# Kernel tuning notes

Hardware: AMD Instinct MI355X
Metric: run time of the kernel (lower is better)

Reference implementation:

```python
import jax, jax.numpy as jnp
import numpy as np

USER_NUM = 100000
ITEM_NUM = 50000
N_NODES = USER_NUM + ITEM_NUM
EMB = 64
NNZ = 6400000
N_LAYERS = 3
NORM_EPS = 1e-12
LEAKY_SLOPE = 0.01
DROP_P = 0.5


def setup_inputs() -> dict:
    key = jax.random.key(0)
    ks = jax.random.split(key, 8)
    return {
        "user_emb": jax.random.normal(ks[0], (USER_NUM, EMB), jnp.float32) * 0.1,
        "item_emb": jax.random.normal(ks[1], (ITEM_NUM, EMB), jnp.float32) * 0.1,
        "image_emb": jax.random.normal(ks[2], (ITEM_NUM, EMB), jnp.float32) * 0.1,
        "text_emb": jax.random.normal(ks[3], (ITEM_NUM, EMB), jnp.float32) * 0.1,
        "fusion_weight": jax.nn.softmax(jax.random.normal(ks[4], (3,), jnp.float32)),
        "adj_vals": jax.random.uniform(ks[5], (NNZ,), jnp.float32) * 0.01,
        "adj_rows": jax.random.randint(ks[6], (NNZ,), 0, N_NODES, jnp.int32),
        "adj_cols": jax.random.randint(ks[7], (NNZ,), 0, N_NODES, jnp.int32),
    }


def _l2norm(x):
    # F.normalize(x, p=2, dim=1) with clamp_min(1e-12)
    n = jnp.sqrt(jnp.sum(x * x, axis=1, keepdims=True))
    return x / jnp.maximum(n, NORM_EPS)


def reference(user_emb, item_emb, image_emb, text_emb, fusion_weight,
              adj_vals, adj_rows, adj_cols):
    def spmm(x):  # COO sparse @ dense: gather cols, scale, scatter-add rows
        return jax.ops.segment_sum(adj_vals[:, None] * x[adj_cols], adj_rows,
                                   num_segments=N_NODES)

    ego = jnp.concatenate([user_emb, item_emb], axis=0)   # [N, E]
    img = jnp.concatenate([user_emb, image_emb], axis=0)  # [N, E]
    txt = jnp.concatenate([user_emb, text_emb], axis=0)   # [N, E]

    dkey = jax.random.key(42)
    ego_acc = jnp.zeros_like(ego)
    img_acc = jnp.zeros_like(img)
    txt_acc = jnp.zeros_like(txt)
    for k in range(N_LAYERS):
        ego = spmm(ego)
        img = spmm(img)
        txt = spmm(txt)
        img = jax.nn.leaky_relu(img, LEAKY_SLOPE)
        txt = jax.nn.leaky_relu(txt, LEAKY_SLOPE)
        ki, kt = jax.random.split(jax.random.fold_in(dkey, k))
        img = jnp.where(jax.random.bernoulli(ki, 1.0 - DROP_P, img.shape),
                        img / (1.0 - DROP_P), 0.0)
        txt = jnp.where(jax.random.bernoulli(kt, 1.0 - DROP_P, txt.shape),
                        txt / (1.0 - DROP_P), 0.0)
        ego_acc = ego_acc + ego
        img_acc = img_acc + _l2norm(img)
        txt_acc = txt_acc + _l2norm(txt)

    inv_l = 1.0 / N_LAYERS
    fin_e = ego_acc * inv_l
    fin_i = img_acc * inv_l
    fin_t = txt_acc * inv_l

    user_all = fin_e[:USER_NUM]
    item_e = fin_e[USER_NUM:]
    item_i = fin_i[USER_NUM:]
    item_t = fin_t[USER_NUM:]
    w = fusion_weight
    item_all = w[0] * item_e + w[1] * item_i + w[2] * item_t
    return user_all, item_all
```

## Files before the change

### kernel.cpp

```cpp
#include <hip/hip_runtime.h>
#include <hip/hip_bf16.h>

#define USER_NUM 100000
#define N_NODES  150000
#define EMB      64
#define NNZ      6400000
#define MATF ((size_t)N_NODES * EMB)

#define RPB1   512
#define NB1    ((N_NODES + RPB1 - 1) / RPB1)
#define CHUNK1 4096
#define NCB    19
#define NCELL  (RPB1 * NCB)

__host__ __device__ __forceinline__ void tf_block(unsigned k0, unsigned k1,
                                                  unsigned x0, unsigned x1,
                                                  unsigned& o0, unsigned& o1) {
    unsigned ks[3] = {k0, k1, k0 ^ k1 ^ 0x1BD11BDAu};
    unsigned X0 = x0 + ks[0];
    unsigned X1 = x1 + ks[1];
    const int R[2][4] = {{13, 15, 26, 6}, {17, 29, 16, 24}};
#pragma unroll
    for (int i = 0; i < 5; ++i) {
        const int* r = R[i & 1];
#pragma unroll
        for (int j = 0; j < 4; ++j) {
            X0 += X1;
            X1 = (X1 << r[j]) | (X1 >> (32 - r[j]));
            X1 ^= X0;
        }
        X0 += ks[(i + 1) % 3];
        X1 += ks[(i + 2) % 3] + (unsigned)(i + 1);
    }
    o0 = X0; o1 = X1;
}

__device__ __forceinline__ unsigned short f_to_bfu(float f) {
    __hip_bfloat16 b = __float2bfloat16(f);
    return *(unsigned short*)&b;
}
__device__ __forceinline__ float bfu_to_f(unsigned short u) {
    return __uint_as_float((unsigned)u << 16);
}

#define BHIST_BLOCKS 2048
__global__ __launch_bounds__(256) void bhist_k(const int* __restrict__ rows,
                                               int* __restrict__ bb) {
    __shared__ int h[NB1];
    for (int i = threadIdx.x; i < NB1; i += 256) h[i] = 0;
    __syncthreads();
    const int stride = BHIST_BLOCKS * 256;
    for (int e = blockIdx.x * 256 + threadIdx.x; e < NNZ; e += stride)
        atomicAdd(&h[rows[e] >> 9], 1);
    __syncthreads();
    for (int i = threadIdx.x; i < NB1; i += 256)
        if (h[i]) atomicAdd(&bb[i], h[i]);
}

__global__ __launch_bounds__(512) void bscan_k(int* __restrict__ bb,
                                               int* __restrict__ bcur) {
    __shared__ int sh[512];
    int t = threadIdx.x;
    int v = (t < NB1) ? bb[t] : 0;
    sh[t] = v;
    __syncthreads();
    for (int off = 1; off < 512; off <<= 1) {
        int x = (t >= off) ? sh[t - off] : 0;
        __syncthreads();
        sh[t] += x;
        __syncthreads();
    }
    int ex = sh[t] - v;
    if (t < NB1) { bb[t] = ex; bcur[t] = ex; }
    if (t == NB1 - 1) bb[NB1] = sh[t];
}

__global__ __launch_bounds__(256) void p1_k(const int* __restrict__ rows,
                                            const int* __restrict__ cols,
                                            const float* __restrict__ vals,
                                            int* __restrict__ bcur,
                                            int2* __restrict__ tmp) {
    __shared__ int2 stage[CHUNK1];
    __shared__ unsigned short sb[CHUNK1];
    __shared__ int hist[NB1], lbase[NB1], lcur[NB1], gbase[NB1];
    const int tid = threadIdx.x;
    const int c0 = blockIdx.x * CHUNK1;
    const int n = (c0 + CHUNK1 <= NNZ) ? CHUNK1 : (NNZ - c0);

    for (int b = tid; b < NB1; b += 256) hist[b] = 0;
    __syncthreads();

    int2 pay[CHUNK1 / 256];
    int  pb[CHUNK1 / 256];
#pragma unroll
    for (int k = 0; k < CHUNK1 / 256; ++k) {
        int i = tid + k * 256;
        if (i < n) {
            int e = c0 + i;
            int r = rows[e];
            int b = r >> 9;
            pay[k] = make_int2(cols[e] | ((r & 511) << 18),
                               __float_as_int(vals[e]));
            pb[k] = b;
            atomicAdd(&hist[b], 1);
        } else pb[k] = -1;
    }
    __syncthreads();

    if (tid == 0) {
        int run = 0;
        for (int b = 0; b < NB1; ++b) {
            lbase[b] = run;
            lcur[b] = run;
            run += hist[b];
        }
    }
    __syncthreads();
    for (int b = tid; b < NB1; b += 256)
        if (hist[b] > 0) gbase[b] = atomicAdd(&bcur[b], hist[b]);
    __syncthreads();

#pragma unroll
    for (int k = 0; k < CHUNK1 / 256; ++k) {
        if (pb[k] >= 0) {
            int pos = atomicAdd(&lcur[pb[k]], 1);
            stage[pos] = pay[k];
            sb[pos] = (unsigned short)pb[k];
        }
    }
    __syncthreads();

    for (int i = tid; i < n; i += 256) {
        int b = sb[i];
        tmp[gbase[b] + (i - lbase[b])] = stage[i];
    }
}

__global__ __launch_bounds__(256) void p2_k(const int* __restrict__ bb,
                                            const int2* __restrict__ tmp,
                                            int2* __restrict__ edges,
                                            int* __restrict__ cur) {
    __shared__ int lh[NCELL];
    __shared__ int ps[256];
    int b = blockIdx.x;
    int tid = threadIdx.x;
    int base = bb[b];
    int cnt = bb[b + 1] - base;

    for (int i = tid; i < NCELL; i += 256) lh[i] = 0;
    __syncthreads();

    for (int i = tid; i < cnt; i += 256) {
        int x = tmp[base + i].x;
        int cell = ((x >> 18) & 511) * NCB + ((x & 0x3FFFF) >> 13);
        atomicAdd(&lh[cell], 1);
    }
    __syncthreads();

    const int PC = (NCELL + 255) / 256;
    int lo = tid * PC;
    int hi = lo + PC < NCELL ? lo + PC : NCELL;
    int s = 0;
    for (int i = lo; i < hi; ++i) s += lh[i];
    ps[tid] = s;
    __syncthreads();
    for (int off = 1; off < 256; off <<= 1) {
        int x = (tid >= off) ? ps[tid - off] : 0;
        __syncthreads();
        ps[tid] += x;
        __syncthreads();
    }
    int run = base + ps[tid] - s;
    for (int i = lo; i < hi; ++i) {
        int d = lh[i];
        lh[i] = run;
        run += d;
    }
    __syncthreads();

    for (int i = tid; i < cnt; i += 256) {
        int2 w = tmp[base + i];
        int cell = ((w.x >> 18) & 511) * NCB + ((w.x & 0x3FFFF) >> 13);
        int pos = atomicAdd(&lh[cell], 1);
        edges[pos] = make_int2(w.x & 0x3FFFF, w.y);
    }
    __syncthreads();

    int r0 = b * RPB1;
    for (int t = tid; t < RPB1; t += 256) {
        int r = r0 + t;
        if (r < N_NODES) cur[r] = lh[t * NCB + (NCB - 1)];
    }
}

__global__ __launch_bounds__(256) void pack0_k(
    const float* __restrict__ user, const float* __restrict__ item,
    const float* __restrict__ image, const float* __restrict__ text,
    unsigned short* __restrict__ pE, unsigned* __restrict__ pIT) {
    size_t idx = (size_t)blockIdx.x * 256 + threadIdx.x;
    if (idx >= MATF) return;
    int row = (int)(idx >> 6);
    float e, i, t;
    if (row < USER_NUM) {
        float u = user[idx];
        e = u; i = u; t = u;
    } else {
        size_t cc = idx - (size_t)USER_NUM * EMB;
        e = item[cc]; i = image[cc]; t = text[cc];
    }
    pE[idx]  = f_to_bfu(e);
    pIT[idx] = (unsigned)f_to_bfu(i) | ((unsigned)f_to_bfu(t) << 16);
}

__global__ __launch_bounds__(256) void spmm_post(
    const int* __restrict__ cur, const int2* __restrict__ edges,
    const unsigned short* __restrict__ sE, const unsigned* __restrict__ sIT,
    unsigned short* __restrict__ dE, unsigned* __restrict__ dIT,
    const float* __restrict__ w, float* __restrict__ out,
    unsigned ki0, unsigned ki1, unsigned kt0, unsigned kt1,
    int writeBack, int first) {
    int row = (int)((blockIdx.x * 256u + threadIdx.x) >> 6);
    int lane = threadIdx.x & 63;
    if (row >= N_NODES) return;
    int beg = __builtin_amdgcn_readfirstlane((row == 0) ? 0 : cur[row - 1]);
    int end = __builtin_amdgcn_readfirstlane(cur[row]);
    float ae = 0.f, ai = 0.f, at = 0.f;
#pragma unroll 8
    for (int i = beg; i < end; ++i) {
        int2 cv = edges[i];
        size_t cc = (size_t)cv.x * EMB + lane;
        float v = __int_as_float(cv.y);
        float xe = bfu_to_f(sE[cc]);
        unsigned it = sIT[cc];
        float xi = __uint_as_float(it << 16);
        float xt = __uint_as_float(it & 0xffff0000u);
        ae += v * xe; ai += v * xi; at += v * xt;
    }

    size_t idx = (size_t)row * EMB + lane;
    unsigned j = (unsigned)idx;

    float iv = ai >= 0.f ? ai : 0.01f * ai;
    float tv = at >= 0.f ? at : 0.01f * at;
    unsigned y0, y1;
    tf_block(ki0, ki1, 0u, j, y0, y1);
    iv = ((y0 ^ y1) >> 31) ? 0.f : iv * 2.f;
    tf_block(kt0, kt1, 0u, j, y0, y1);
    tv = ((y0 ^ y1) >> 31) ? 0.f : tv * 2.f;

    if (writeBack) {
        dE[idx]  = f_to_bfu(ae);
        dIT[idx] = (unsigned)f_to_bfu(iv) | ((unsigned)f_to_bfu(tv) << 16);
    }

    float si = iv * iv, st2 = tv * tv;
#pragma unroll
    for (int m = 1; m < 64; m <<= 1) {
        si  += __shfl_xor(si, m, 64);
        st2 += __shfl_xor(st2, m, 64);
    }
    float ni = iv / fmaxf(sqrtf(si), 1e-12f);
    float nt = tv / fmaxf(sqrtf(st2), 1e-12f);

    const float inv3 = 1.0f / 3.0f;
    float contrib = (row < USER_NUM) ? ae * inv3
                                     : (w[0] * ae + w[1] * ni + w[2] * nt) * inv3;
    if (first) out[idx] = contrib;
    else       out[idx] += contrib;
}

extern "C" void kernel_launch(void* const* d_in, const int* in_sizes, int n_in,
                              void* d_out, int out_size, void* d_ws, size_t ws_size,
                              hipStream_t stream) {
    const float* user  = (const float*)d_in[0];
    const float* item  = (const float*)d_in[1];
    const float* image = (const float*)d_in[2];
    const float* text  = (const float*)d_in[3];
    const float* w     = (const float*)d_in[4];
    const float* vals  = (const float*)d_in[5];
    const int*   rows  = (const int*)d_in[6];
    const int*   cols  = (const int*)d_in[7];
    float* out = (float*)d_out;

    int2* edges = (int2*)d_ws;
    unsigned short* eA = (unsigned short*)(edges + NNZ);
    unsigned short* eB = eA + MATF;
    unsigned* itA = (unsigned*)(eB + MATF);
    unsigned* itB = itA + MATF;
    int* cur  = (int*)(itB + MATF);
    int* bb   = cur + N_NODES;
    int* bcur = bb + (NB1 + 2);
    int2* tmp = (int2*)eB;

    hipMemsetAsync(bb, 0, (NB1 + 1) * sizeof(int), stream);
    bhist_k<<<BHIST_BLOCKS, 256, 0, stream>>>(rows, bb);
    bscan_k<<<1, 512, 0, stream>>>(bb, bcur);
    p1_k<<<(NNZ + CHUNK1 - 1) / CHUNK1, 256, 0, stream>>>(rows, cols, vals,
                                                          bcur, tmp);
    p2_k<<<NB1, 256, 0, stream>>>(bb, tmp, edges, cur);

    const int blocks = (int)((MATF + 255) / 256);
    pack0_k<<<blocks, 256, 0, stream>>>(user, item, image, text, eA, itA);

    unsigned short* sE = eA; unsigned* sIT = itA;
    unsigned short* dE = eB; unsigned* dIT = itB;
    for (int k = 0; k < 3; ++k) {
        unsigned f0, f1, a0, a1, b0, b1;
        tf_block(0u, 42u, 0u, (unsigned)k, f0, f1);
        tf_block(f0, f1, 0u, 0u, a0, a1);
        tf_block(f0, f1, 0u, 1u, b0, b1);
        int writeBack = (k < 2) ? 1 : 0;
        spmm_post<<<blocks, 256, 0, stream>>>(
            cur, edges, sE, sIT, dE, dIT, w, out, a0, a1, b0, b1,
            writeBack, k == 0 ? 1 : 0);
        unsigned short* te = sE; unsigned* tit = sIT;
        sE = dE; sIT = dIT;
        dE = te; dIT = tit;
    }
}
```

Baseline: 1.280 ms.

## Pack user and item inputs separately and add non-temporal edge/output accesses

The initial packing no longer builds concatenated ego/img/txt matrices. It stores the user rows once plus separate item, image and text buffers. The first SpMM layer is specialised to branch per column: a user column is gathered once into a single accumulator that is later added to all three channels. Edge loads and output and writeback stores become non-temporal hints to reduce cache pollution. The changes add a data-dependent branch in the first-layer inner loop and extra workspace, and the non-temporal hints may hurt if the data would have been reused.

After: 1.349 ms. 1.05x slower.

```diff
diff --git a/kernel.cpp b/kernel.cpp
--- a/kernel.cpp
+++ b/kernel.cpp
@@ -6,6 +6,8 @@
 #define EMB      64
 #define NNZ      6400000
 #define MATF ((size_t)N_NODES * EMB)
+#define UMATF ((size_t)USER_NUM * EMB)
+#define IMATF ((size_t)(N_NODES - USER_NUM) * EMB)
 
 #define RPB1   512
 #define NB1    ((N_NODES + RPB1 - 1) / RPB1)
@@ -196,46 +198,62 @@
 __global__ __launch_bounds__(256) void pack0_k(
     const float* __restrict__ user, const float* __restrict__ item,
     const float* __restrict__ image, const float* __restrict__ text,
-    unsigned short* __restrict__ pE, unsigned* __restrict__ pIT) {
+    unsigned short* __restrict__ pU, unsigned short* __restrict__ pIE,
+    unsigned* __restrict__ pIIT) {
     size_t idx = (size_t)blockIdx.x * 256 + threadIdx.x;
-    if (idx >= MATF) return;
-    int row = (int)(idx >> 6);
-    float e, i, t;
-    if (row < USER_NUM) {
-        float u = user[idx];
-        e = u; i = u; t = u;
-    } else {
-        size_t cc = idx - (size_t)USER_NUM * EMB;
-        e = item[cc]; i = image[cc]; t = text[cc];
-    }
-    pE[idx]  = f_to_bfu(e);
-    pIT[idx] = (unsigned)f_to_bfu(i) | ((unsigned)f_to_bfu(t) << 16);
-}
-
+    if (idx < UMATF) {
+        pU[idx] = f_to_bfu(user[idx]);
+    }
+    if (idx < IMATF) {
+        pIE[idx]  = f_to_bfu(item[idx]);
+        pIIT[idx] = (unsigned)f_to_bfu(image[idx]) |
+                    ((unsigned)f_to_bfu(text[idx]) << 16);
+    }
+}
+
+template <bool FIRST>
 __global__ __launch_bounds__(256) void spmm_post(
     const int* __restrict__ cur, const int2* __restrict__ edges,
     const unsigned short* __restrict__ sE, const unsigned* __restrict__ sIT,
+    const unsigned short* __restrict__ pU, const unsigned short* __restrict__ pIE,
+    const unsigned* __restrict__ pIIT,
     unsigned short* __restrict__ dE, unsigned* __restrict__ dIT,
     const float* __restrict__ w, float* __restrict__ out,
-    unsigned ki0, unsigned ki1, unsigned kt0, unsigned kt1,
-    int writeBack, int first) {
+    unsigned ki0, unsigned ki1, unsigned kt0, unsigned kt1, int writeBack) {
     int row = (int)((blockIdx.x * 256u + threadIdx.x) >> 6);
     int lane = threadIdx.x & 63;
     if (row >= N_NODES) return;
     int beg = __builtin_amdgcn_readfirstlane((row == 0) ? 0 : cur[row - 1]);
     int end = __builtin_amdgcn_readfirstlane(cur[row]);
-    float ae = 0.f, ai = 0.f, at = 0.f;
+    const long long* edges64 = (const long long*)edges;
+    float ae = 0.f, ai = 0.f, at = 0.f, su = 0.f;
 #pragma unroll 8
     for (int i = beg; i < end; ++i) {
-        int2 cv = edges[i];
-        size_t cc = (size_t)cv.x * EMB + lane;
-        float v = __int_as_float(cv.y);
-        float xe = bfu_to_f(sE[cc]);
-        unsigned it = sIT[cc];
-        float xi = __uint_as_float(it << 16);
-        float xt = __uint_as_float(it & 0xffff0000u);
-        ae += v * xe; ai += v * xi; at += v * xt;
-    }
+        long long cvp = __builtin_nontemporal_load(edges64 + i);
+        int c = (int)(unsigned)(cvp & 0xffffffffu);
+        float v = __uint_as_float((unsigned)((unsigned long long)cvp >> 32));
+        if (FIRST) {
+            if (c < USER_NUM) {
+                float u = bfu_to_f(pU[(size_t)c * EMB + lane]);
+                su += v * u;
+            } else {
+                size_t cc = (size_t)(c - USER_NUM) * EMB + lane;
+                float xe = bfu_to_f(pIE[cc]);
+                unsigned it = pIIT[cc];
+                ae += v * xe;
+                ai += v * __uint_as_float(it << 16);
+                at += v * __uint_as_float(it & 0xffff0000u);
+            }
+        } else {
+            size_t cc = (size_t)c * EMB + lane;
+            float xe = bfu_to_f(sE[cc]);
+            unsigned it = sIT[cc];
+            ae += v * xe;
+            ai += v * __uint_as_float(it << 16);
+            at += v * __uint_as_float(it & 0xffff0000u);
+        }
+    }
+    if (FIRST) { ae += su; ai += su; at += su; }
 
     size_t idx = (size_t)row * EMB + lane;
     unsigned j = (unsigned)idx;
@@ -249,8 +267,9 @@
     tv = ((y0 ^ y1) >> 31) ? 0.f : tv * 2.f;
 
     if (writeBack) {
-        dE[idx]  = f_to_bfu(ae);
-        dIT[idx] = (unsigned)f_to_bfu(iv) | ((unsigned)f_to_bfu(tv) << 16);
+        __builtin_nontemporal_store(f_to_bfu(ae), &dE[idx]);
+        __builtin_nontemporal_store(
+            (unsigned)f_to_bfu(iv) | ((unsigned)f_to_bfu(tv) << 16), &dIT[idx]);
     }
 
     float si = iv * iv, st2 = tv * tv;
@@ -265,8 +284,12 @@
     const float inv3 = 1.0f / 3.0f;
     float contrib = (row < USER_NUM) ? ae * inv3
                                      : (w[0] * ae + w[1] * ni + w[2] * nt) * inv3;
-    if (first) out[idx] = contrib;
-    else       out[idx] += contrib;
+    if (FIRST) {
+        __builtin_nontemporal_store(contrib, &out[idx]);
+    } else {
+        float o = __builtin_nontemporal_load(&out[idx]);
+        __builtin_nontemporal_store(o + contrib, &out[idx]);
+    }
 }
 
 extern "C" void kernel_launch(void* const* d_in, const int* in_sizes, int n_in,
@@ -287,7 +310,10 @@
     unsigned short* eB = eA + MATF;
     unsigned* itA = (unsigned*)(eB + MATF);
     unsigned* itB = itA + MATF;
-    int* cur  = (int*)(itB + MATF);
+    unsigned short* pU  = (unsigned short*)(itB + MATF);
+    unsigned short* pIE = pU + UMATF;
+    unsigned* pIIT = (unsigned*)(pIE + IMATF);
+    int* cur  = (int*)(pIIT + IMATF);
     int* bb   = cur + N_NODES;
     int* bcur = bb + (NB1 + 2);
     int2* tmp = (int2*)eB;
@@ -300,21 +326,26 @@
     p2_k<<<NB1, 256, 0, stream>>>(bb, tmp, edges, cur);
 
     const int blocks = (int)((MATF + 255) / 256);
-    pack0_k<<<blocks, 256, 0, stream>>>(user, item, image, text, eA, itA);
-
-    unsigned short* sE = eA; unsigned* sIT = itA;
-    unsigned short* dE = eB; unsigned* dIT = itB;
+    pack0_k<<<(int)((UMATF + 255) / 256), 256, 0, stream>>>(
+        user, item, image, text, pU, pIE, pIIT);
+
     for (int k = 0; k < 3; ++k) {
         unsigned f0, f1, a0, a1, b0, b1;
         tf_block(0u, 42u, 0u, (unsigned)k, f0, f1);
         tf_block(f0, f1, 0u, 0u, a0, a1);
         tf_block(f0, f1, 0u, 1u, b0, b1);
-        int writeBack = (k < 2) ? 1 : 0;
-        spmm_post<<<blocks, 256, 0, stream>>>(
-            cur, edges, sE, sIT, dE, dIT, w, out, a0, a1, b0, b1,
-            writeBack, k == 0 ? 1 : 0);
-        unsigned short* te = sE; unsigned* tit = sIT;
-        sE = dE; sIT = dIT;
-        dE = te; dIT = tit;
-    }
-}
+        if (k == 0) {
+            spmm_post<true><<<blocks, 256, 0, stream>>>(
+                cur, edges, nullptr, nullptr, pU, pIE, pIIT,
+                eA, itA, w, out, a0, a1, b0, b1, 1);
+        } else if (k == 1) {
+            spmm_post<false><<<blocks, 256, 0, stream>>>(
+                cur, edges, eA, itA, nullptr, nullptr, nullptr,
+                eB, itB, w, out, a0, a1, b0, b1, 1);
+        } else {
+            spmm_post<false><<<blocks, 256, 0, stream>>>(
+                cur, edges, eB, itB, nullptr, nullptr, nullptr,
+                nullptr, nullptr, w, out, a0, a1, b0, b1, 0);
+        }
+    }
+}
```
